# Performance work log

Measured on AMD Instinct MI355X. Metric: run time of the kernel, lower is better.

## Reference

```python
import jax, jax.numpy as jnp
import numpy as np


def _rnn_scan(x_pre, W_hh, b_hh, h0):
    # x_pre: [S, B, H] precomputed input projection; returns stacked h: [S, B, H]
    def step(h, xp):
        h = jnp.tanh(xp + h @ W_hh.T + b_hh)
        return h, h
    _, hs = jax.lax.scan(step, h0, x_pre)
    return hs


def setup_inputs() -> dict:
    key = jax.random.key(0)
    ks = jax.random.split(key, 12)
    B, S, E, H, V = 16, 256, 512, 1024, 32000
    sE, sH = 1.0 / np.sqrt(E), 1.0 / np.sqrt(H)
    return {
        "x_ids": jax.random.randint(ks[0], (B, S), 0, V),
        "emb": jax.random.normal(ks[1], (V, E), jnp.float32),
        "W_ih1": jax.random.normal(ks[2], (H, E), jnp.float32) * sE,
        "b_ih1": jax.random.normal(ks[3], (H,), jnp.float32) * sH,
        "W_hh1": jax.random.normal(ks[4], (H, H), jnp.float32) * sH,
        "b_hh1": jax.random.normal(ks[5], (H,), jnp.float32) * sH,
        "W_ih2": jax.random.normal(ks[6], (H, H), jnp.float32) * sH,
        "b_ih2": jax.random.normal(ks[7], (H,), jnp.float32) * sH,
        "W_hh2": jax.random.normal(ks[8], (H, H), jnp.float32) * sH,
        "b_hh2": jax.random.normal(ks[9], (H,), jnp.float32) * sH,
        "W_fc": jax.random.normal(ks[10], (V, H), jnp.float32) * sH,
        "b_fc": jax.random.normal(ks[11], (V,), jnp.float32) * sH,
    }


def reference(x_ids, emb, W_ih1, b_ih1, W_hh1, b_hh1, W_ih2, b_ih2, W_hh2, b_hh2, W_fc, b_fc):
    B, S = x_ids.shape
    H = W_hh1.shape[0]
    x = emb[x_ids]  # [B, S, E]
    # layer 1: precompute input projection for all steps, scan over time
    x1 = jnp.einsum('bse,he->sbh', x, W_ih1) + b_ih1  # [S, B, H]
    h0 = jnp.zeros((B, H), x.dtype)
    h1s = _rnn_scan(x1, W_hh1, b_hh1, h0)  # [S, B, H]
    # layer 2
    x2 = jnp.einsum('sbh,gh->sbg', h1s, W_ih2) + b_ih2
    h2s = _rnn_scan(x2, W_hh2, b_hh2, h0)  # [S, B, H]
    # per-step fc + softmax, vectorized
    logits = jnp.einsum('sbh,vh->bsv', h2s, W_fc) + b_fc  # [B, S, V]
    return jax.nn.softmax(logits, axis=-1)
```

## Files before the change

### kernel.cpp

```cpp
#include <hip/hip_runtime.h>
#include <cstdint>
#include <cstddef>

typedef unsigned short u16;
typedef __attribute__((ext_vector_type(4))) float f32x4;
typedef __attribute__((ext_vector_type(8))) short s16x8;
typedef __attribute__((ext_vector_type(8))) unsigned short u16x8;
typedef __attribute__((ext_vector_type(4))) unsigned short u16x4;

#define B_ 16
#define S_ 256
#define E_ 512
#define H_ 1024
#define V_ 32000
#define M_TOK (S_*B_)
#define BH (B_*H_)

__device__ __forceinline__ u16 f2bf(float f) {
  union { float f; unsigned u; } x; x.f = f;
  unsigned r = x.u + 0x7fffu + ((x.u >> 16) & 1u);
  return (u16)(r >> 16);
}
__device__ __forceinline__ float bf2f(u16 x) {
  union { unsigned u; float f; } c; c.u = ((unsigned)x) << 16; return c.f;
}

__device__ __forceinline__ void sc_load16(s16x8& d, const u16* p) {
  asm volatile("global_load_dwordx4 %0, %1, off sc0 sc1" : "=v"(d) : "v"(p));
}
__device__ __forceinline__ void sc_load8w(u16x4& d, const u16* p) {
  asm volatile("global_load_dwordx2 %0, %1, off sc0 sc1\n\ts_waitcnt vmcnt(0)"
               : "=v"(d) : "v"(p) : "memory");
}
__device__ __forceinline__ int sc_load4w(const int* p) {
  int d;
  asm volatile("global_load_dword %0, %1, off sc0 sc1\n\ts_waitcnt vmcnt(0)"
               : "=v"(d) : "v"(p) : "memory");
  return d;
}
__device__ __forceinline__ void sc_store8(u16* p, u16x4 v) {
  asm volatile("global_store_dwordx2 %0, %1, off sc0 sc1" :: "v"(p), "v"(v) : "memory");
}
__device__ __forceinline__ void sc_store4(int* p, int v) {
  asm volatile("global_store_dword %0, %1, off sc0 sc1" :: "v"(p), "v"(v) : "memory");
}
__device__ __forceinline__ void wait_vm0() {
  asm volatile("s_waitcnt vmcnt(0)" ::: "memory");
}

__global__ __launch_bounds__(256) void k_cvt(const float* __restrict__ src,
                                             u16* __restrict__ dst, int n4) {
  int i = blockIdx.x*blockDim.x + threadIdx.x;
  int stride = gridDim.x*blockDim.x;
  for (; i < n4; i += stride) {
    float4 v = reinterpret_cast<const float4*>(src)[i];
    ushort4 o;
    o.x = f2bf(v.x); o.y = f2bf(v.y); o.z = f2bf(v.z); o.w = f2bf(v.w);
    reinterpret_cast<ushort4*>(dst)[i] = o;
  }
}

__global__ __launch_bounds__(256) void k_embed(const int* __restrict__ ids,
                                               const float* __restrict__ emb,
                                               u16* __restrict__ A1) {
  int g = blockIdx.x*256 + threadIdx.x;
  int m = g >> 6;
  int c = g & 63;
  int s = m >> 4, b = m & 15;
  int id = ids[b*S_ + s];
  const float4* src = reinterpret_cast<const float4*>(emb + (size_t)id*E_ + (size_t)c*8);
  float4 v0 = src[0], v1 = src[1];
  u16x8 o;
  o[0]=f2bf(v0.x); o[1]=f2bf(v0.y); o[2]=f2bf(v0.z); o[3]=f2bf(v0.w);
  o[4]=f2bf(v1.x); o[5]=f2bf(v1.y); o[6]=f2bf(v1.z); o[7]=f2bf(v1.w);
  *reinterpret_cast<u16x8*>(A1 + (size_t)m*E_ + (size_t)c*8) = o;
}

#define BM 128
#define BN 128
#define BK 32

__device__ __forceinline__ void gload_lds16(const u16* g, u16* l) {
  __builtin_amdgcn_global_load_lds(
      (const __attribute__((address_space(1))) void*)g,
      (__attribute__((address_space(3))) void*)l,
      16, 0, 0);
}

template<int FCMODE>
__global__ __launch_bounds__(256)
void k_gemm(const u16* __restrict__ A, const u16* __restrict__ Bw,
            float* __restrict__ C, const float* __restrict__ bias,
            int M, int N, int K)
{
  __shared__ u16 lA[2][BM*BK];
  __shared__ u16 lB[2][BN*BK];
  const int tid = threadIdx.x;
  const int l = tid & 63, w = tid >> 6;

  const int nwg = gridDim.x * gridDim.y;
  int d = blockIdx.y * gridDim.x + blockIdx.x;
  int tt = (d & 7) * (nwg >> 3) + (d >> 3);
  const int n0 = (tt / gridDim.y) * BN;
  const int m0 = (tt % gridDim.y) * BM;

  const int wr = w >> 1, wc = w & 1;

  const int L0 = (w*2+0)*64 + l;
  const int L1 = (w*2+1)*64 + l;
  const int r0 = L0 >> 2, r1 = L1 >> 2;
  const int c0 = (L0 & 3) ^ ((r0 >> 1) & 3);
  const int c1 = (L1 & 3) ^ ((r1 >> 1) & 3);
  const u16* gA0 = A  + (size_t)(m0 + r0)*K + c0*8;
  const u16* gA1 = A  + (size_t)(m0 + r1)*K + c1*8;
  const u16* gB0 = Bw + (size_t)(n0 + r0)*K + c0*8;
  const u16* gB1 = Bw + (size_t)(n0 + r1)*K + c1*8;

  const int fr = l & 15;
  const int xc = (l >> 4) ^ ((fr >> 1) & 3);
  int aoff[4], boff[4];
#pragma unroll
  for (int f = 0; f < 4; ++f) {
    aoff[f] = (wr*64 + f*16 + fr) * BK + xc*8;
    boff[f] = (wc*64 + f*16 + fr) * BK + xc*8;
  }

  f32x4 acc[4][4] = {};
  const int KT = K / BK;

  gload_lds16(gA0, &lA[0][(w*2+0)*512]);
  gload_lds16(gA1, &lA[0][(w*2+1)*512]);
  gload_lds16(gB0, &lB[0][(w*2+0)*512]);
  gload_lds16(gB1, &lB[0][(w*2+1)*512]);
  __syncthreads();

  for (int kt = 0; kt < KT; ++kt) {
    const int buf = kt & 1;
    if (kt + 1 < KT) {
      const int koff = (kt+1)*BK;
      gload_lds16(gA0 + koff, &lA[buf^1][(w*2+0)*512]);
      gload_lds16(gA1 + koff, &lA[buf^1][(w*2+1)*512]);
      gload_lds16(gB0 + koff, &lB[buf^1][(w*2+0)*512]);
      gload_lds16(gB1 + koff, &lB[buf^1][(w*2+1)*512]);
    }
    s16x8 af[4], bq[4];
#pragma unroll
    for (int f = 0; f < 4; ++f) af[f] = *reinterpret_cast<const s16x8*>(&lA[buf][aoff[f]]);
#pragma unroll
    for (int f = 0; f < 4; ++f) bq[f] = *reinterpret_cast<const s16x8*>(&lB[buf][boff[f]]);
#pragma unroll
    for (int fm = 0; fm < 4; ++fm)
#pragma unroll
      for (int fn = 0; fn < 4; ++fn)
        acc[fm][fn] = __builtin_amdgcn_mfma_f32_16x16x32_bf16(af[fm], bq[fn], acc[fm][fn], 0, 0, 0);
    __syncthreads();
  }

  const int rowb = (l >> 4) * 4;
  const int colb = l & 15;
#pragma unroll
  for (int fm = 0; fm < 4; ++fm) {
#pragma unroll
    for (int fn = 0; fn < 4; ++fn) {
      const int col = n0 + wc*64 + fn*16 + colb;
#pragma unroll
      for (int r = 0; r < 4; ++r) {
        const int row = m0 + wr*64 + fm*16 + rowb + r;
        float v = acc[fm][fn][r];
        if (FCMODE == 1) {
          const int b = row & 15, s = row >> 4;
          C[((size_t)(b*S_ + s))*N + col] = v + bias[col];
        } else if (FCMODE == 2) {
          ((u16*)C)[(size_t)row*N + col] = f2bf(v);
        } else {
          C[(size_t)row*N + col] = v;
        }
      }
    }
  }
}

__global__ __launch_bounds__(256, 1)
void k_scan5(const u16* __restrict__ Whh1, const u16* __restrict__ Wih2,
             const u16* __restrict__ Whh2, const u16* __restrict__ x1b,
             const float* __restrict__ bih1, const float* __restrict__ bhh1,
             const float* __restrict__ bih2, const float* __restrict__ bhh2,
             u16* __restrict__ h1s, u16* __restrict__ u2s, u16* __restrict__ h2s,
             int* __restrict__ s1, int* __restrict__ su, int* __restrict__ s2)
{
  __shared__ u16 sh[BH];
  const int tid = threadIdx.x;
  const int l = tid & 63, w = tid >> 6;
  const int role = blockIdx.x >> 4;
  const int blk  = blockIdx.x & 15;
  const int rowA = blk*64 + w*16 + (l & 15);
  const int kc = l >> 4;
  const int bcol = l & 15;
  const int i0 = blk*64 + w*16 + kc*4;
  const int jme = (tid & 127) >> 3;

  const u16* Wsel = (role == 0) ? Whh1 : (role == 1) ? Wih2 : Whh2;
  s16x8 wf[32];
  {
    const u16* wp = Wsel + (size_t)rowA*H_ + kc*8;
#pragma unroll
    for (int ks = 0; ks < 32; ++ks) wf[ks] = *reinterpret_cast<const s16x8*>(wp + ks*32);
  }

  auto stage = [&](const u16* src, const int* sentrow) {
    while (sc_load4w(sentrow + jme) != 0) __builtin_amdgcn_s_sleep(2);
    s16x8 stg[8];
#pragma unroll
    for (int r = 0; r < 8; ++r) sc_load16(stg[r], src + (size_t)(tid + r*256)*8);
    wait_vm0();
#pragma unroll
    for (int r = 0; r < 8; ++r) {
      int idx8 = tid + r*256;
      int bt = idx8 >> 7, c8 = idx8 & 127;
      *reinterpret_cast<s16x8*>(reinterpret_cast<char*>(sh) +
          bt*2048 + ((c8*16) ^ ((bt & 7) << 4))) = stg[r];
    }
  };

  const int swz = (bcol & 7) << 4;
  auto hfrag = [&](int ks) -> s16x8 {
    return *reinterpret_cast<const s16x8*>(
        reinterpret_cast<const char*>(sh) + bcol*2048 + (((kc*16) + ks*64) ^ swz));
  };
  auto mfma32 = [&](f32x4& a0, f32x4& a1, f32x4& a2, f32x4& a3) {
#pragma unroll
    for (int ks = 0; ks < 32; ks += 4) {
      a0 = __builtin_amdgcn_mfma_f32_16x16x32_bf16(wf[ks+0], hfrag(ks+0), a0, 0, 0, 0);
      a1 = __builtin_amdgcn_mfma_f32_16x16x32_bf16(wf[ks+1], hfrag(ks+1), a1, 0, 0, 0);
      a2 = __builtin_amdgcn_mfma_f32_16x16x32_bf16(wf[ks+2], hfrag(ks+2), a2, 0, 0, 0);
      a3 = __builtin_amdgcn_mfma_f32_16x16x32_bf16(wf[ks+3], hfrag(ks+3), a3, 0, 0, 0);
    }
  };

  if (role == 0) {
    float bc[4];
#pragma unroll
    for (int r = 0; r < 4; ++r) bc[r] = bih1[i0+r] + bhh1[i0+r];
    for (int t = 0; t < S_; ++t) {
      f32x4 a0 = {}, a1 = {}, a2 = {}, a3 = {};
      if (t > 0) {
        stage(h1s + (size_t)(t-1)*BH, s1 + (t-1)*16);
        __syncthreads();
        mfma32(a0, a1, a2, a3);
      }
      u16x4 xr = *reinterpret_cast<const u16x4*>(x1b + (size_t)(t*B_ + bcol)*H_ + i0);
      f32x4 tot = (a0 + a1) + (a2 + a3);
      u16x4 o;
      o[0] = f2bf(tanhf(tot[0] + bf2f(xr[0]) + bc[0]));
      o[1] = f2bf(tanhf(tot[1] + bf2f(xr[1]) + bc[1]));
      o[2] = f2bf(tanhf(tot[2] + bf2f(xr[2]) + bc[2]));
      o[3] = f2bf(tanhf(tot[3] + bf2f(xr[3]) + bc[3]));
      sc_store8(h1s + (size_t)(t*B_ + bcol)*H_ + i0, o);
      wait_vm0();
      __syncthreads();
      if (tid == 0) sc_store4(s1 + t*16 + blk, 0);
    }
  } else if (role == 1) {
    float bc[4];
#pragma unroll
    for (int r = 0; r < 4; ++r) bc[r] = bih2[i0+r] + bhh2[i0+r];
    for (int t = 0; t < S_; ++t) {
      stage(h1s + (size_t)t*BH, s1 + t*16);
      __syncthreads();
      f32x4 a0 = {}, a1 = {}, a2 = {}, a3 = {};
      mfma32(a0, a1, a2, a3);
      f32x4 tot = (a0 + a1) + (a2 + a3);
      u16x4 o;
      o[0] = f2bf(tot[0] + bc[0]);
      o[1] = f2bf(tot[1] + bc[1]);
      o[2] = f2bf(tot[2] + bc[2]);
      o[3] = f2bf(tot[3] + bc[3]);
      sc_store8(u2s + (size_t)(t*B_ + bcol)*H_ + i0, o);
      wait_vm0();
      __syncthreads();
      if (tid == 0) sc_store4(su + t*16 + blk, 0);
    }
  } else {
    for (int t = 0; t < S_; ++t) {
      if (tid == 0) {
        while (sc_load4w(su + t*16 + blk) != 0) __builtin_amdgcn_s_sleep(2);
      }
      if (t > 0) stage(h2s + (size_t)(t-1)*BH, s2 + (t-1)*16);
      __syncthreads();
      u16x4 uv;
      sc_load8w(uv, u2s + (size_t)(t*B_ + bcol)*H_ + i0);
      f32x4 a0 = {}, a1 = {}, a2 = {}, a3 = {};
      if (t > 0) mfma32(a0, a1, a2, a3);
      f32x4 tot = (a0 + a1) + (a2 + a3);
      u16x4 o;
      o[0] = f2bf(tanhf(tot[0] + bf2f(uv[0])));
      o[1] = f2bf(tanhf(tot[1] + bf2f(uv[1])));
      o[2] = f2bf(tanhf(tot[2] + bf2f(uv[2])));
      o[3] = f2bf(tanhf(tot[3] + bf2f(uv[3])));
      sc_store8(h2s + (size_t)(t*B_ + bcol)*H_ + i0, o);
      wait_vm0();
      __syncthreads();
      if (tid == 0) sc_store4(s2 + t*16 + blk, 0);
    }
  }
}

__global__ __launch_bounds__(256)
void k_softmax(float* __restrict__ out) {
  const int gw = (blockIdx.x*256 + threadIdx.x) >> 6;
  const int l = threadIdx.x & 63;
  float* row = out + (size_t)gw*V_;
  float m = -3.4e38f, s = 0.f;
  for (int it = 0; it < 125; ++it) {
    float4 v = reinterpret_cast<const float4*>(row)[it*64 + l];
    float cm = fmaxf(fmaxf(v.x, v.y), fmaxf(v.z, v.w));
    float nm = fmaxf(m, cm);
    s = s*__expf(m - nm) + __expf(v.x-nm) + __expf(v.y-nm) + __expf(v.z-nm) + __expf(v.w-nm);
    m = nm;
  }
#pragma unroll
  for (int o = 32; o; o >>= 1) {
    float m2 = __shfl_xor(m, o), s2 = __shfl_xor(s, o);
    float nm = fmaxf(m, m2);
    s = s*__expf(m - nm) + s2*__expf(m2 - nm);
    m = nm;
  }
  const float inv = 1.f / s;
  for (int it = 0; it < 125; ++it) {
    float4 v = reinterpret_cast<const float4*>(row)[it*64 + l];
    float4 p;
    p.x = __expf(v.x - m)*inv; p.y = __expf(v.y - m)*inv;
    p.z = __expf(v.z - m)*inv; p.w = __expf(v.w - m)*inv;
    reinterpret_cast<float4*>(row)[it*64 + l] = p;
  }
}

extern "C" void kernel_launch(void* const* d_in, const int* in_sizes, int n_in,
                              void* d_out, int out_size, void* d_ws, size_t ws_size,
                              hipStream_t stream) {
  (void)in_sizes; (void)n_in; (void)out_size; (void)ws_size;
  const int*   x_ids = (const int*)  d_in[0];
  const float* emb   = (const float*)d_in[1];
  const float* Wih1  = (const float*)d_in[2];
  const float* bih1  = (const float*)d_in[3];
  const float* Whh1  = (const float*)d_in[4];
  const float* bhh1  = (const float*)d_in[5];
  const float* Wih2  = (const float*)d_in[6];
  const float* bih2  = (const float*)d_in[7];
  const float* Whh2  = (const float*)d_in[8];
  const float* bhh2  = (const float*)d_in[9];
  const float* Wfc   = (const float*)d_in[10];
  const float* bfc   = (const float*)d_in[11];
  float* out = (float*)d_out;

  char* ws = (char*)d_ws;
  size_t off = 0;
  auto alloc = [&](size_t bytes) {
    char* p = ws + off; off += (bytes + 255) & ~(size_t)255; return p;
  };
  int* sent   = (int*) alloc(3 * S_ * 16 * 4);
  u16* Wfcb   = (u16*) alloc((size_t)V_*H_*2);
  u16* Whh1b  = (u16*) alloc((size_t)H_*H_*2);
  u16* Wih2b  = (u16*) alloc((size_t)H_*H_*2);
  u16* Whh2b  = (u16*) alloc((size_t)H_*H_*2);
  u16* x1b    = (u16*) alloc((size_t)M_TOK*H_*2);
  u16* h1s    = (u16*) alloc((size_t)M_TOK*H_*2);
  u16* u2s    = (u16*) alloc((size_t)M_TOK*H_*2);
  u16* h2s    = (u16*) alloc((size_t)M_TOK*H_*2);
  u16* A1     = (u16*) alloc((size_t)M_TOK*E_*2);
  u16* Wih1b  = (u16*) alloc((size_t)H_*E_*2);
  int* s1 = sent, *su = sent + S_*16, *s2 = sent + 2*S_*16;

  k_cvt<<<256,  256, 0, stream>>>(Wih1, Wih1b, H_*E_/4);
  k_cvt<<<256,  256, 0, stream>>>(Whh1, Whh1b, H_*H_/4);
  k_cvt<<<256,  256, 0, stream>>>(Wih2, Wih2b, H_*H_/4);
  k_cvt<<<256,  256, 0, stream>>>(Whh2, Whh2b, H_*H_/4);
  k_cvt<<<2048, 256, 0, stream>>>(Wfc,  Wfcb,  V_*H_/4);
  k_embed<<<M_TOK*64/256, 256, 0, stream>>>(x_ids, emb, A1);

  k_gemm<2><<<dim3(H_/BN, M_TOK/BM), 256, 0, stream>>>(A1, Wih1b, (float*)x1b, nullptr, M_TOK, H_, E_);

  hipMemsetAsync(sent, 0xFF, 3 * S_ * 16 * 4, stream);
  k_scan5<<<48, 256, 0, stream>>>(Whh1b, Wih2b, Whh2b, x1b,
                                  bih1, bhh1, bih2, bhh2,
                                  h1s, u2s, h2s, s1, su, s2);

  k_gemm<1><<<dim3(V_/BN, M_TOK/BM), 256, 0, stream>>>(h2s, Wfcb, out, bfc, M_TOK, V_, H_);
  k_softmax<<<M_TOK/4, 256, 0, stream>>>(out);
}
```

Measured before the change: 1.935 ms.

## Use poisoned hidden-state data as flags and load fragments straight into registers

Drops the separate per-step sentinel arrays in the fused scan kernel. The h1/u2/h2 buffers are pre-filled with 0xFF, so every lane polls its own MFMA B-fragments straight from global memory until no all-ones dword remains. This removes the LDS staging, the block barriers, the vmcnt waits after each store and the flag stores from the serial per-timestep critical path. In exchange it adds three large memsets before the scan. Each wave now reads the full previous hidden state on its own, which multiplies L2 traffic per block.

```diff
diff --git a/kernel.cpp b/kernel.cpp
--- a/kernel.cpp
+++ b/kernel.cpp
@@ -7,6 +7,8 @@
 typedef __attribute__((ext_vector_type(8))) short s16x8;
 typedef __attribute__((ext_vector_type(8))) unsigned short u16x8;
 typedef __attribute__((ext_vector_type(4))) unsigned short u16x4;
+typedef __attribute__((ext_vector_type(4))) unsigned u32x4;
+typedef __attribute__((ext_vector_type(2))) unsigned u32x2;
 
 #define B_ 16
 #define S_ 256
@@ -25,24 +27,15 @@
   union { unsigned u; float f; } c; c.u = ((unsigned)x) << 16; return c.f;
 }
 
-__device__ __forceinline__ void sc_load16(s16x8& d, const u16* p) {
+__device__ __forceinline__ void sc_load16u(u32x4& d, const u16* p) {
   asm volatile("global_load_dwordx4 %0, %1, off sc0 sc1" : "=v"(d) : "v"(p));
 }
-__device__ __forceinline__ void sc_load8w(u16x4& d, const u16* p) {
+__device__ __forceinline__ void sc_load8u(u32x2& d, const u16* p) {
   asm volatile("global_load_dwordx2 %0, %1, off sc0 sc1\n\ts_waitcnt vmcnt(0)"
                : "=v"(d) : "v"(p) : "memory");
 }
-__device__ __forceinline__ int sc_load4w(const int* p) {
-  int d;
-  asm volatile("global_load_dword %0, %1, off sc0 sc1\n\ts_waitcnt vmcnt(0)"
-               : "=v"(d) : "v"(p) : "memory");
-  return d;
-}
 __device__ __forceinline__ void sc_store8(u16* p, u16x4 v) {
   asm volatile("global_store_dwordx2 %0, %1, off sc0 sc1" :: "v"(p), "v"(v) : "memory");
-}
-__device__ __forceinline__ void sc_store4(int* p, int v) {
-  asm volatile("global_store_dword %0, %1, off sc0 sc1" :: "v"(p), "v"(v) : "memory");
 }
 __device__ __forceinline__ void wait_vm0() {
   asm volatile("s_waitcnt vmcnt(0)" ::: "memory");
@@ -181,14 +174,12 @@
 }
 
 __global__ __launch_bounds__(256, 1)
-void k_scan5(const u16* __restrict__ Whh1, const u16* __restrict__ Wih2,
+void k_scan6(const u16* __restrict__ Whh1, const u16* __restrict__ Wih2,
              const u16* __restrict__ Whh2, const u16* __restrict__ x1b,
              const float* __restrict__ bih1, const float* __restrict__ bhh1,
              const float* __restrict__ bih2, const float* __restrict__ bhh2,
-             u16* __restrict__ h1s, u16* __restrict__ u2s, u16* __restrict__ h2s,
-             int* __restrict__ s1, int* __restrict__ su, int* __restrict__ s2)
+             u16* __restrict__ h1s, u16* __restrict__ u2s, u16* __restrict__ h2s)
 {
-  __shared__ u16 sh[BH];
   const int tid = threadIdx.x;
   const int l = tid & 63, w = tid >> 6;
   const int role = blockIdx.x >> 4;
@@ -197,7 +188,6 @@
   const int kc = l >> 4;
   const int bcol = l & 15;
   const int i0 = blk*64 + w*16 + kc*4;
-  const int jme = (tid & 127) >> 3;
 
   const u16* Wsel = (role == 0) ? Whh1 : (role == 1) ? Wih2 : Whh2;
   s16x8 wf[32];
@@ -207,33 +197,40 @@
     for (int ks = 0; ks < 32; ++ks) wf[ks] = *reinterpret_cast<const s16x8*>(wp + ks*32);
   }
 
-  auto stage = [&](const u16* src, const int* sentrow) {
-    while (sc_load4w(sentrow + jme) != 0) __builtin_amdgcn_s_sleep(2);
-    s16x8 stg[8];
-#pragma unroll
-    for (int r = 0; r < 8; ++r) sc_load16(stg[r], src + (size_t)(tid + r*256)*8);
+  u32x4 hf[32];
+
+  auto pollfrags = [&](const u16* hrow) {
+#pragma unroll
+    for (int ks = 0; ks < 32; ++ks) sc_load16u(hf[ks], hrow + ks*32);
     wait_vm0();
-#pragma unroll
-    for (int r = 0; r < 8; ++r) {
-      int idx8 = tid + r*256;
-      int bt = idx8 >> 7, c8 = idx8 & 127;
-      *reinterpret_cast<s16x8*>(reinterpret_cast<char*>(sh) +
-          bt*2048 + ((c8*16) ^ ((bt & 7) << 4))) = stg[r];
+    for (;;) {
+      unsigned M = 0;
+#pragma unroll
+      for (int ks = 0; ks < 32; ++ks) {
+        unsigned m0 = hf[ks][0] > hf[ks][1] ? hf[ks][0] : hf[ks][1];
+        unsigned m1 = hf[ks][2] > hf[ks][3] ? hf[ks][2] : hf[ks][3];
+        unsigned mm = m0 > m1 ? m0 : m1;
+        M = mm > M ? mm : M;
+      }
+      if (!__any(M == 0xFFFFFFFFu)) break;
+#pragma unroll
+      for (int ks = 0; ks < 32; ++ks) {
+        unsigned m0 = hf[ks][0] > hf[ks][1] ? hf[ks][0] : hf[ks][1];
+        unsigned m1 = hf[ks][2] > hf[ks][3] ? hf[ks][2] : hf[ks][3];
+        unsigned mm = m0 > m1 ? m0 : m1;
+        if (mm == 0xFFFFFFFFu) sc_load16u(hf[ks], hrow + ks*32);
+      }
+      wait_vm0();
     }
   };
 
-  const int swz = (bcol & 7) << 4;
-  auto hfrag = [&](int ks) -> s16x8 {
-    return *reinterpret_cast<const s16x8*>(
-        reinterpret_cast<const char*>(sh) + bcol*2048 + (((kc*16) + ks*64) ^ swz));
-  };
   auto mfma32 = [&](f32x4& a0, f32x4& a1, f32x4& a2, f32x4& a3) {
 #pragma unroll
     for (int ks = 0; ks < 32; ks += 4) {
-      a0 = __builtin_amdgcn_mfma_f32_16x16x32_bf16(wf[ks+0], hfrag(ks+0), a0, 0, 0, 0);
-      a1 = __builtin_amdgcn_mfma_f32_16x16x32_bf16(wf[ks+1], hfrag(ks+1), a1, 0, 0, 0);
-      a2 = __builtin_amdgcn_mfma_f32_16x16x32_bf16(wf[ks+2], hfrag(ks+2), a2, 0, 0, 0);
-      a3 = __builtin_amdgcn_mfma_f32_16x16x32_bf16(wf[ks+3], hfrag(ks+3), a3, 0, 0, 0);
+      a0 = __builtin_amdgcn_mfma_f32_16x16x32_bf16(wf[ks+0], __builtin_bit_cast(s16x8, hf[ks+0]), a0, 0, 0, 0);
+      a1 = __builtin_amdgcn_mfma_f32_16x16x32_bf16(wf[ks+1], __builtin_bit_cast(s16x8, hf[ks+1]), a1, 0, 0, 0);
+      a2 = __builtin_amdgcn_mfma_f32_16x16x32_bf16(wf[ks+2], __builtin_bit_cast(s16x8, hf[ks+2]), a2, 0, 0, 0);
+      a3 = __builtin_amdgcn_mfma_f32_16x16x32_bf16(wf[ks+3], __builtin_bit_cast(s16x8, hf[ks+3]), a3, 0, 0, 0);
     }
   };
 
@@ -242,13 +239,12 @@
 #pragma unroll
     for (int r = 0; r < 4; ++r) bc[r] = bih1[i0+r] + bhh1[i0+r];
     for (int t = 0; t < S_; ++t) {
+      u16x4 xr = *reinterpret_cast<const u16x4*>(x1b + (size_t)(t*B_ + bcol)*H_ + i0);
       f32x4 a0 = {}, a1 = {}, a2 = {}, a3 = {};
       if (t > 0) {
-        stage(h1s + (size_t)(t-1)*BH, s1 + (t-1)*16);
-        __syncthreads();
+        pollfrags(h1s + ((size_t)(t-1)*B_ + bcol)*H_ + kc*8);
         mfma32(a0, a1, a2, a3);
       }
-      u16x4 xr = *reinterpret_cast<const u16x4*>(x1b + (size_t)(t*B_ + bcol)*H_ + i0);
       f32x4 tot = (a0 + a1) + (a2 + a3);
       u16x4 o;
       o[0] = f2bf(tanhf(tot[0] + bf2f(xr[0]) + bc[0]));
@@ -256,17 +252,13 @@
       o[2] = f2bf(tanhf(tot[2] + bf2f(xr[2]) + bc[2]));
       o[3] = f2bf(tanhf(tot[3] + bf2f(xr[3]) + bc[3]));
       sc_store8(h1s + (size_t)(t*B_ + bcol)*H_ + i0, o);
-      wait_vm0();
-      __syncthreads();
-      if (tid == 0) sc_store4(s1 + t*16 + blk, 0);
     }
   } else if (role == 1) {
     float bc[4];
 #pragma unroll
     for (int r = 0; r < 4; ++r) bc[r] = bih2[i0+r] + bhh2[i0+r];
     for (int t = 0; t < S_; ++t) {
-      stage(h1s + (size_t)t*BH, s1 + t*16);
-      __syncthreads();
+      pollfrags(h1s + ((size_t)t*B_ + bcol)*H_ + kc*8);
       f32x4 a0 = {}, a1 = {}, a2 = {}, a3 = {};
       mfma32(a0, a1, a2, a3);
       f32x4 tot = (a0 + a1) + (a2 + a3);
@@ -276,31 +268,26 @@
       o[2] = f2bf(tot[2] + bc[2]);
       o[3] = f2bf(tot[3] + bc[3]);
       sc_store8(u2s + (size_t)(t*B_ + bcol)*H_ + i0, o);
-      wait_vm0();
-      __syncthreads();
-      if (tid == 0) sc_store4(su + t*16 + blk, 0);
     }
   } else {
     for (int t = 0; t < S_; ++t) {
-      if (tid == 0) {
-        while (sc_load4w(su + t*16 + blk) != 0) __builtin_amdgcn_s_sleep(2);
-      }
-      if (t > 0) stage(h2s + (size_t)(t-1)*BH, s2 + (t-1)*16);
-      __syncthreads();
-      u16x4 uv;
-      sc_load8w(uv, u2s + (size_t)(t*B_ + bcol)*H_ + i0);
+      const u16* up = u2s + (size_t)(t*B_ + bcol)*H_ + i0;
       f32x4 a0 = {}, a1 = {}, a2 = {}, a3 = {};
+      if (t > 0) {
+        pollfrags(h2s + ((size_t)(t-1)*B_ + bcol)*H_ + kc*8);
+      }
+      u32x2 uv;
+      sc_load8u(uv, up);
+      while ((uv[0] > uv[1] ? uv[0] : uv[1]) == 0xFFFFFFFFu) sc_load8u(uv, up);
+      u16x4 uq = __builtin_bit_cast(u16x4, uv);
       if (t > 0) mfma32(a0, a1, a2, a3);
       f32x4 tot = (a0 + a1) + (a2 + a3);
       u16x4 o;
-      o[0] = f2bf(tanhf(tot[0] + bf2f(uv[0])));
-      o[1] = f2bf(tanhf(tot[1] + bf2f(uv[1])));
-      o[2] = f2bf(tanhf(tot[2] + bf2f(uv[2])));
-      o[3] = f2bf(tanhf(tot[3] + bf2f(uv[3])));
+      o[0] = f2bf(tanhf(tot[0] + bf2f(uq[0])));
+      o[1] = f2bf(tanhf(tot[1] + bf2f(uq[1])));
+      o[2] = f2bf(tanhf(tot[2] + bf2f(uq[2])));
+      o[3] = f2bf(tanhf(tot[3] + bf2f(uq[3])));
       sc_store8(h2s + (size_t)(t*B_ + bcol)*H_ + i0, o);
-      wait_vm0();
-      __syncthreads();
-      if (tid == 0) sc_store4(s2 + t*16 + blk, 0);
     }
   }
 }
@@ -358,7 +345,6 @@
   auto alloc = [&](size_t bytes) {
     char* p = ws + off; off += (bytes + 255) & ~(size_t)255; return p;
   };
-  int* sent   = (int*) alloc(3 * S_ * 16 * 4);
   u16* Wfcb   = (u16*) alloc((size_t)V_*H_*2);
   u16* Whh1b  = (u16*) alloc((size_t)H_*H_*2);
   u16* Wih2b  = (u16*) alloc((size_t)H_*H_*2);
@@ -369,7 +355,6 @@
   u16* h2s    = (u16*) alloc((size_t)M_TOK*H_*2);
   u16* A1     = (u16*) alloc((size_t)M_TOK*E_*2);
   u16* Wih1b  = (u16*) alloc((size_t)H_*E_*2);
-  int* s1 = sent, *su = sent + S_*16, *s2 = sent + 2*S_*16;
 
   k_cvt<<<256,  256, 0, stream>>>(Wih1, Wih1b, H_*E_/4);
   k_cvt<<<256,  256, 0, stream>>>(Whh1, Whh1b, H_*H_/4);
@@ -380,10 +365,11 @@
 
   k_gemm<2><<<dim3(H_/BN, M_TOK/BM), 256, 0, stream>>>(A1, Wih1b, (float*)x1b, nullptr, M_TOK, H_, E_);
 
-  hipMemsetAsync(sent, 0xFF, 3 * S_ * 16 * 4, stream);
-  k_scan5<<<48, 256, 0, stream>>>(Whh1b, Wih2b, Whh2b, x1b,
-                                  bih1, bhh1, bih2, bhh2,
-                                  h1s, u2s, h2s, s1, su, s2);
+  hipMemsetAsync(h1s, 0xFF, (size_t)M_TOK*H_*2, stream);
+  hipMemsetAsync(u2s, 0xFF, (size_t)M_TOK*H_*2, stream);
+  hipMemsetAsync(h2s, 0xFF, (size_t)M_TOK*H_*2, stream);
+  k_scan6<<<48, 256, 0, stream>>>(Whh1b, Wih2b, Whh2b, x1b,
+                                  bih1, bhh1, bih2, bhh2, h1s, u2s, h2s);
 
   k_gemm<1><<<dim3(V_/BN, M_TOK/BM), 256, 0, stream>>>(h2s, Wfcb, out, bfc, M_TOK, V_, H_);
   k_softmax<<<M_TOK/4, 256, 0, stream>>>(out);
```

Measured after the change: 2.503 ms. 29.3% more time.

## Overlap FC GEMM tiles with RNN scan in a persistent megakernel

Applied to the files above, without the earlier changes.

Merges the recurrent scan and the output FC GEMM into one launch. The 48 scan blocks publish per-block progress of layer 2, and the FC tile blocks wait on that progress with a bounded spin before computing their tile, so the FC work can run on idle CUs while the scan is still going. Tiles that time out are marked not done and are recomputed by a cleanup kernel. This risks FC blocks taking CU slots or memory bandwidth from the scan blocks, adds spin-wait traffic, and relies on the scan blocks being scheduled first, since block dispatch order is not guaranteed.

```diff
diff --git a/kernel.cpp b/kernel.cpp
--- a/kernel.cpp
+++ b/kernel.cpp
@@ -7,6 +7,7 @@
 typedef __attribute__((ext_vector_type(8))) short s16x8;
 typedef __attribute__((ext_vector_type(8))) unsigned short u16x8;
 typedef __attribute__((ext_vector_type(4))) unsigned short u16x4;
+typedef __attribute__((ext_vector_type(4))) unsigned u32x4;
 
 #define B_ 16
 #define S_ 256
@@ -15,6 +16,8 @@
 #define V_ 32000
 #define M_TOK (S_*B_)
 #define BH (B_*H_)
+#define NT_FC 250
+#define MT_FC 32
 
 __device__ __forceinline__ u16 f2bf(float f) {
   union { float f; unsigned u; } x; x.f = f;
@@ -26,6 +29,9 @@
 }
 
 __device__ __forceinline__ void sc_load16(s16x8& d, const u16* p) {
+  asm volatile("global_load_dwordx4 %0, %1, off sc0 sc1" : "=v"(d) : "v"(p));
+}
+__device__ __forceinline__ void sc_load16u(u32x4& d, const u16* p) {
   asm volatile("global_load_dwordx4 %0, %1, off sc0 sc1" : "=v"(d) : "v"(p));
 }
 __device__ __forceinline__ void sc_load8w(u16x4& d, const u16* p) {
@@ -167,10 +173,7 @@
       for (int r = 0; r < 4; ++r) {
         const int row = m0 + wr*64 + fm*16 + rowb + r;
         float v = acc[fm][fn][r];
-        if (FCMODE == 1) {
-          const int b = row & 15, s = row >> 4;
-          C[((size_t)(b*S_ + s))*N + col] = v + bias[col];
-        } else if (FCMODE == 2) {
+        if (FCMODE == 2) {
           ((u16*)C)[(size_t)row*N + col] = f2bf(v);
         } else {
           C[(size_t)row*N + col] = v;
@@ -180,129 +183,267 @@
   }
 }
 
-__global__ __launch_bounds__(256, 1)
-void k_scan5(const u16* __restrict__ Whh1, const u16* __restrict__ Wih2,
-             const u16* __restrict__ Whh2, const u16* __restrict__ x1b,
-             const float* __restrict__ bih1, const float* __restrict__ bhh1,
-             const float* __restrict__ bih2, const float* __restrict__ bhh2,
-             u16* __restrict__ h1s, u16* __restrict__ u2s, u16* __restrict__ h2s,
-             int* __restrict__ s1, int* __restrict__ su, int* __restrict__ s2)
+__device__ __forceinline__ void fc_tile(const u16* __restrict__ A, const u16* __restrict__ Bw,
+                                        float* __restrict__ C, const float* __restrict__ bias,
+                                        int m0, int n0, u16* smem)
 {
-  __shared__ u16 sh[BH];
   const int tid = threadIdx.x;
   const int l = tid & 63, w = tid >> 6;
-  const int role = blockIdx.x >> 4;
-  const int blk  = blockIdx.x & 15;
-  const int rowA = blk*64 + w*16 + (l & 15);
-  const int kc = l >> 4;
-  const int bcol = l & 15;
-  const int i0 = blk*64 + w*16 + kc*4;
-  const int jme = (tid & 127) >> 3;
-
-  const u16* Wsel = (role == 0) ? Whh1 : (role == 1) ? Wih2 : Whh2;
-  s16x8 wf[32];
-  {
-    const u16* wp = Wsel + (size_t)rowA*H_ + kc*8;
-#pragma unroll
-    for (int ks = 0; ks < 32; ++ks) wf[ks] = *reinterpret_cast<const s16x8*>(wp + ks*32);
-  }
-
-  auto stage = [&](const u16* src, const int* sentrow) {
-    while (sc_load4w(sentrow + jme) != 0) __builtin_amdgcn_s_sleep(2);
-    s16x8 stg[8];
-#pragma unroll
-    for (int r = 0; r < 8; ++r) sc_load16(stg[r], src + (size_t)(tid + r*256)*8);
-    wait_vm0();
-#pragma unroll
-    for (int r = 0; r < 8; ++r) {
-      int idx8 = tid + r*256;
-      int bt = idx8 >> 7, c8 = idx8 & 127;
-      *reinterpret_cast<s16x8*>(reinterpret_cast<char*>(sh) +
-          bt*2048 + ((c8*16) ^ ((bt & 7) << 4))) = stg[r];
-    }
-  };
-
-  const int swz = (bcol & 7) << 4;
-  auto hfrag = [&](int ks) -> s16x8 {
-    return *reinterpret_cast<const s16x8*>(
-        reinterpret_cast<const char*>(sh) + bcol*2048 + (((kc*16) + ks*64) ^ swz));
-  };
-  auto mfma32 = [&](f32x4& a0, f32x4& a1, f32x4& a2, f32x4& a3) {
-#pragma unroll
-    for (int ks = 0; ks < 32; ks += 4) {
-      a0 = __builtin_amdgcn_mfma_f32_16x16x32_bf16(wf[ks+0], hfrag(ks+0), a0, 0, 0, 0);
-      a1 = __builtin_amdgcn_mfma_f32_16x16x32_bf16(wf[ks+1], hfrag(ks+1), a1, 0, 0, 0);
-      a2 = __builtin_amdgcn_mfma_f32_16x16x32_bf16(wf[ks+2], hfrag(ks+2), a2, 0, 0, 0);
-      a3 = __builtin_amdgcn_mfma_f32_16x16x32_bf16(wf[ks+3], hfrag(ks+3), a3, 0, 0, 0);
-    }
-  };
-
-  if (role == 0) {
-    float bc[4];
-#pragma unroll
-    for (int r = 0; r < 4; ++r) bc[r] = bih1[i0+r] + bhh1[i0+r];
-    for (int t = 0; t < S_; ++t) {
-      f32x4 a0 = {}, a1 = {}, a2 = {}, a3 = {};
-      if (t > 0) {
-        stage(h1s + (size_t)(t-1)*BH, s1 + (t-1)*16);
+  const int wr = w >> 1, wc = w & 1;
+  u16* lA = smem;
+  u16* lB = smem + 8192;
+
+  const int L0 = (w*2+0)*64 + l;
+  const int L1 = (w*2+1)*64 + l;
+  const int r0 = L0 >> 2, r1 = L1 >> 2;
+  const int c0 = (L0 & 3) ^ ((r0 >> 1) & 3);
+  const int c1 = (L1 & 3) ^ ((r1 >> 1) & 3);
+  const u16* gA0 = A  + (size_t)(m0 + r0)*H_ + c0*8;
+  const u16* gA1 = A  + (size_t)(m0 + r1)*H_ + c1*8;
+  const u16* gB0 = Bw + (size_t)(n0 + r0)*H_ + c0*8;
+  const u16* gB1 = Bw + (size_t)(n0 + r1)*H_ + c1*8;
+
+  const int fr = l & 15;
+  const int xc = (l >> 4) ^ ((fr >> 1) & 3);
+  int aoff[4], boff[4];
+#pragma unroll
+  for (int f = 0; f < 4; ++f) {
+    aoff[f] = (wr*64 + f*16 + fr) * BK + xc*8;
+    boff[f] = (wc*64 + f*16 + fr) * BK + xc*8;
+  }
+
+  f32x4 acc[4][4] = {};
+
+  gload_lds16(gA0, lA + (w*2+0)*512);
+  gload_lds16(gA1, lA + (w*2+1)*512);
+  gload_lds16(gB0, lB + (w*2+0)*512);
+  gload_lds16(gB1, lB + (w*2+1)*512);
+  __syncthreads();
+
+  for (int kt = 0; kt < 32; ++kt) {
+    const int buf = kt & 1;
+    if (kt + 1 < 32) {
+      const int koff = (kt+1)*BK;
+      gload_lds16(gA0 + koff, lA + (buf^1)*4096 + (w*2+0)*512);
+      gload_lds16(gA1 + koff, lA + (buf^1)*4096 + (w*2+1)*512);
+      gload_lds16(gB0 + koff, lB + (buf^1)*4096 + (w*2+0)*512);
+      gload_lds16(gB1 + koff, lB + (buf^1)*4096 + (w*2+1)*512);
+    }
+    s16x8 af[4], bq[4];
+#pragma unroll
+    for (int f = 0; f < 4; ++f) af[f] = *reinterpret_cast<const s16x8*>(lA + buf*4096 + aoff[f]);
+#pragma unroll
+    for (int f = 0; f < 4; ++f) bq[f] = *reinterpret_cast<const s16x8*>(lB + buf*4096 + boff[f]);
+#pragma unroll
+    for (int fm = 0; fm < 4; ++fm)
+#pragma unroll
+      for (int fn = 0; fn < 4; ++fn)
+        acc[fm][fn] = __builtin_amdgcn_mfma_f32_16x16x32_bf16(af[fm], bq[fn], acc[fm][fn], 0, 0, 0);
+    __syncthreads();
+  }
+
+  const int rowb = (l >> 4) * 4;
+  const int colb = l & 15;
+#pragma unroll
+  for (int fm = 0; fm < 4; ++fm) {
+#pragma unroll
+    for (int fn = 0; fn < 4; ++fn) {
+      const int col = n0 + wc*64 + fn*16 + colb;
+      const float bv = bias[col];
+#pragma unroll
+      for (int r = 0; r < 4; ++r) {
+        const int row = m0 + wr*64 + fm*16 + rowb + r;
+        const int b = row & 15, s = row >> 4;
+        C[((size_t)(b*S_ + s))*V_ + col] = acc[fm][fn][r] + bv;
+      }
+    }
+  }
+}
+
+__global__ __launch_bounds__(256)
+void k_mega(const u16* __restrict__ Whh1, const u16* __restrict__ Wih2,
+            const u16* __restrict__ Whh2, const u16* __restrict__ x1b,
+            const float* __restrict__ bih1, const float* __restrict__ bhh1,
+            const float* __restrict__ bih2, const float* __restrict__ bhh2,
+            u16* __restrict__ h1s, u16* __restrict__ u2s, u16* __restrict__ h2s,
+            int* __restrict__ s1, int* __restrict__ su, int* __restrict__ s2,
+            const u16* __restrict__ Wfcb, const float* __restrict__ bfc,
+            float* __restrict__ out, int* __restrict__ prog2, int* __restrict__ done)
+{
+  __shared__ u16 smem[16384];
+  const int bid = blockIdx.x;
+  const int tid = threadIdx.x;
+
+  if (bid < 48) {
+    const int l = tid & 63, w = tid >> 6;
+    const int role = bid >> 4;
+    const int blk  = bid & 15;
+    const int rowA = blk*64 + w*16 + (l & 15);
+    const int kc = l >> 4;
+    const int bcol = l & 15;
+    const int i0 = blk*64 + w*16 + kc*4;
+    const int jme = (tid & 127) >> 3;
+
+    const u16* Wsel = (role == 0) ? Whh1 : (role == 1) ? Wih2 : Whh2;
+    s16x8 wf[32];
+    {
+      const u16* wp = Wsel + (size_t)rowA*H_ + kc*8;
+#pragma unroll
+      for (int ks = 0; ks < 32; ++ks) wf[ks] = *reinterpret_cast<const s16x8*>(wp + ks*32);
+    }
+
+    auto stage = [&](const u16* src, const int* sentrow) {
+      while (sc_load4w(sentrow + jme) != 0) __builtin_amdgcn_s_sleep(2);
+      s16x8 stg[8];
+#pragma unroll
+      for (int r = 0; r < 8; ++r) sc_load16(stg[r], src + (size_t)(tid + r*256)*8);
+      wait_vm0();
+#pragma unroll
+      for (int r = 0; r < 8; ++r) {
+        int idx8 = tid + r*256;
+        int bt = idx8 >> 7, c8 = idx8 & 127;
+        *reinterpret_cast<s16x8*>(reinterpret_cast<char*>(smem) +
+            bt*2048 + ((c8*16) ^ ((bt & 7) << 4))) = stg[r];
+      }
+    };
+
+    const int swz = (bcol & 7) << 4;
+    auto hfrag = [&](int ks) -> s16x8 {
+      return *reinterpret_cast<const s16x8*>(
+          reinterpret_cast<const char*>(smem) + bcol*2048 + (((kc*16) + ks*64) ^ swz));
+    };
+    auto mfma32 = [&](f32x4& a0, f32x4& a1, f32x4& a2, f32x4& a3) {
+#pragma unroll
+      for (int ks = 0; ks < 32; ks += 4) {
+        a0 = __builtin_amdgcn_mfma_f32_16x16x32_bf16(wf[ks+0], hfrag(ks+0), a0, 0, 0, 0);
+        a1 = __builtin_amdgcn_mfma_f32_16x16x32_bf16(wf[ks+1], hfrag(ks+1), a1, 0, 0, 0);
+        a2 = __builtin_amdgcn_mfma_f32_16x16x32_bf16(wf[ks+2], hfrag(ks+2), a2, 0, 0, 0);
+        a3 = __builtin_amdgcn_mfma_f32_16x16x32_bf16(wf[ks+3], hfrag(ks+3), a3, 0, 0, 0);
+      }
+    };
+
+    if (role == 0) {
+      float bc[4];
+#pragma unroll
+      for (int r = 0; r < 4; ++r) bc[r] = bih1[i0+r] + bhh1[i0+r];
+      for (int t = 0; t < S_; ++t) {
+        f32x4 a0 = {}, a1 = {}, a2 = {}, a3 = {};
+        if (t > 0) {
+          stage(h1s + (size_t)(t-1)*BH, s1 + (t-1)*16);
+          __syncthreads();
+          mfma32(a0, a1, a2, a3);
+        }
+        u16x4 xr = *reinterpret_cast<const u16x4*>(x1b + (size_t)(t*B_ + bcol)*H_ + i0);
+        f32x4 tot = (a0 + a1) + (a2 + a3);
+        u16x4 o;
+        o[0] = f2bf(tanhf(tot[0] + bf2f(xr[0]) + bc[0]));
+        o[1] = f2bf(tanhf(tot[1] + bf2f(xr[1]) + bc[1]));
+        o[2] = f2bf(tanhf(tot[2] + bf2f(xr[2]) + bc[2]));
+        o[3] = f2bf(tanhf(tot[3] + bf2f(xr[3]) + bc[3]));
+        sc_store8(h1s + (size_t)(t*B_ + bcol)*H_ + i0, o);
+        wait_vm0();
         __syncthreads();
+        if (tid == 0) sc_store4(s1 + t*16 + blk, 0);
+      }
+    } else if (role == 1) {
+      float bc[4];
+#pragma unroll
+      for (int r = 0; r < 4; ++r) bc[r] = bih2[i0+r] + bhh2[i0+r];
+      for (int t = 0; t < S_; ++t) {
+        stage(h1s + (size_t)t*BH, s1 + t*16);
+        __syncthreads();
+        f32x4 a0 = {}, a1 = {}, a2 = {}, a3 = {};
         mfma32(a0, a1, a2, a3);
-      }
-      u16x4 xr = *reinterpret_cast<const u16x4*>(x1b + (size_t)(t*B_ + bcol)*H_ + i0);
-      f32x4 tot = (a0 + a1) + (a2 + a3);
-      u16x4 o;
-      o[0] = f2bf(tanhf(tot[0] + bf2f(xr[0]) + bc[0]));
-      o[1] = f2bf(tanhf(tot[1] + bf2f(xr[1]) + bc[1]));
-      o[2] = f2bf(tanhf(tot[2] + bf2f(xr[2]) + bc[2]));
-      o[3] = f2bf(tanhf(tot[3] + bf2f(xr[3]) + bc[3]));
-      sc_store8(h1s + (size_t)(t*B_ + bcol)*H_ + i0, o);
+        f32x4 tot = (a0 + a1) + (a2 + a3);
+        u16x4 o;
+        o[0] = f2bf(tot[0] + bc[0]);
+        o[1] = f2bf(tot[1] + bc[1]);
+        o[2] = f2bf(tot[2] + bc[2]);
+        o[3] = f2bf(tot[3] + bc[3]);
+        sc_store8(u2s + (size_t)(t*B_ + bcol)*H_ + i0, o);
+        wait_vm0();
+        __syncthreads();
+        if (tid == 0) sc_store4(su + t*16 + blk, 0);
+      }
+    } else {
+      for (int t = 0; t < S_; ++t) {
+        if (tid == 0) {
+          while (sc_load4w(su + t*16 + blk) != 0) __builtin_amdgcn_s_sleep(2);
+        }
+        if (t > 0) stage(h2s + (size_t)(t-1)*BH, s2 + (t-1)*16);
+        __syncthreads();
+        u16x4 uv;
+        sc_load8w(uv, u2s + (size_t)(t*B_ + bcol)*H_ + i0);
+        f32x4 a0 = {}, a1 = {}, a2 = {}, a3 = {};
+        if (t > 0) mfma32(a0, a1, a2, a3);
+        f32x4 tot = (a0 + a1) + (a2 + a3);
+        u16x4 o;
+        o[0] = f2bf(tanhf(tot[0] + bf2f(uv[0])));
+        o[1] = f2bf(tanhf(tot[1] + bf2f(uv[1])));
+        o[2] = f2bf(tanhf(tot[2] + bf2f(uv[2])));
+        o[3] = f2bf(tanhf(tot[3] + bf2f(uv[3])));
+        sc_store8(h2s + (size_t)(t*B_ + bcol)*H_ + i0, o);
+        wait_vm0();
+        __syncthreads();
+        if (tid == 0) {
+          sc_store4(s2 + t*16 + blk, 0);
+          sc_store4(prog2 + blk, t + 1);
+        }
+      }
+    }
+    return;
+  }
+
+  const int q = bid - 48;
+  if (q >= MT_FC * NT_FC) return;
+  const int mt = q / NT_FC;
+  const int nt = q - mt * NT_FC;
+  const unsigned need = (unsigned)((mt + 1) * 8);
+
+  __shared__ int s_ok;
+  if (tid == 0) {
+    int ok = 0;
+    const u16* pp = (const u16*)prog2;
+    for (int it = 0; it < 2500; ++it) {
+      u32x4 pa, pb, pc, pd;
+      sc_load16u(pa, pp); sc_load16u(pb, pp + 8);
+      sc_load16u(pc, pp + 16); sc_load16u(pd, pp + 24);
       wait_vm0();
-      __syncthreads();
-      if (tid == 0) sc_store4(s1 + t*16 + blk, 0);
-    }
-  } else if (role == 1) {
-    float bc[4];
-#pragma unroll
-    for (int r = 0; r < 4; ++r) bc[r] = bih2[i0+r] + bhh2[i0+r];
-    for (int t = 0; t < S_; ++t) {
-      stage(h1s + (size_t)t*BH, s1 + t*16);
-      __syncthreads();
-      f32x4 a0 = {}, a1 = {}, a2 = {}, a3 = {};
-      mfma32(a0, a1, a2, a3);
-      f32x4 tot = (a0 + a1) + (a2 + a3);
-      u16x4 o;
-      o[0] = f2bf(tot[0] + bc[0]);
-      o[1] = f2bf(tot[1] + bc[1]);
-      o[2] = f2bf(tot[2] + bc[2]);
-      o[3] = f2bf(tot[3] + bc[3]);
-      sc_store8(u2s + (size_t)(t*B_ + bcol)*H_ + i0, o);
-      wait_vm0();
-      __syncthreads();
-      if (tid == 0) sc_store4(su + t*16 + blk, 0);
-    }
-  } else {
-    for (int t = 0; t < S_; ++t) {
-      if (tid == 0) {
-        while (sc_load4w(su + t*16 + blk) != 0) __builtin_amdgcn_s_sleep(2);
-      }
-      if (t > 0) stage(h2s + (size_t)(t-1)*BH, s2 + (t-1)*16);
-      __syncthreads();
-      u16x4 uv;
-      sc_load8w(uv, u2s + (size_t)(t*B_ + bcol)*H_ + i0);
-      f32x4 a0 = {}, a1 = {}, a2 = {}, a3 = {};
-      if (t > 0) mfma32(a0, a1, a2, a3);
-      f32x4 tot = (a0 + a1) + (a2 + a3);
-      u16x4 o;
-      o[0] = f2bf(tanhf(tot[0] + bf2f(uv[0])));
-      o[1] = f2bf(tanhf(tot[1] + bf2f(uv[1])));
-      o[2] = f2bf(tanhf(tot[2] + bf2f(uv[2])));
-      o[3] = f2bf(tanhf(tot[3] + bf2f(uv[3])));
-      sc_store8(h2s + (size_t)(t*B_ + bcol)*H_ + i0, o);
-      wait_vm0();
-      __syncthreads();
-      if (tid == 0) sc_store4(s2 + t*16 + blk, 0);
-    }
-  }
+      unsigned m0 = pa[0] < pa[1] ? pa[0] : pa[1];
+      unsigned m1 = pa[2] < pa[3] ? pa[2] : pa[3];
+      unsigned m2 = pb[0] < pb[1] ? pb[0] : pb[1];
+      unsigned m3 = pb[2] < pb[3] ? pb[2] : pb[3];
+      unsigned m4 = pc[0] < pc[1] ? pc[0] : pc[1];
+      unsigned m5 = pc[2] < pc[3] ? pc[2] : pc[3];
+      unsigned m6 = pd[0] < pd[1] ? pd[0] : pd[1];
+      unsigned m7 = pd[2] < pd[3] ? pd[2] : pd[3];
+      m0 = m0 < m1 ? m0 : m1;  m2 = m2 < m3 ? m2 : m3;
+      m4 = m4 < m5 ? m4 : m5;  m6 = m6 < m7 ? m6 : m7;
+      m0 = m0 < m2 ? m0 : m2;  m4 = m4 < m6 ? m4 : m6;
+      unsigned mn = m0 < m4 ? m0 : m4;
+      if (mn >= need) { ok = 1; break; }
+      __builtin_amdgcn_s_sleep(32);
+    }
+    s_ok = ok;
+  }
+  __syncthreads();
+  if (!s_ok) return;
+
+  fc_tile(h2s, Wfcb, out, bfc, mt*BM, nt*BN, smem);
+  if (tid == 0) done[q] = 1;
+}
+
+__global__ __launch_bounds__(256)
+void k_fc_cleanup(const u16* __restrict__ h2s, const u16* __restrict__ Wfcb,
+                  const float* __restrict__ bfc, float* __restrict__ out,
+                  const int* __restrict__ done)
+{
+  __shared__ u16 smem[16384];
+  const int q = blockIdx.x;
+  if (done[q]) return;
+  const int mt = q / NT_FC;
+  const int nt = q - mt * NT_FC;
+  fc_tile(h2s, Wfcb, out, bfc, mt*BM, nt*BN, smem);
 }
 
 __global__ __launch_bounds__(256)
@@ -359,6 +500,7 @@
     char* p = ws + off; off += (bytes + 255) & ~(size_t)255; return p;
   };
   int* sent   = (int*) alloc(3 * S_ * 16 * 4);
+  int* ctrl   = (int*) alloc(64 + MT_FC*NT_FC*4);
   u16* Wfcb   = (u16*) alloc((size_t)V_*H_*2);
   u16* Whh1b  = (u16*) alloc((size_t)H_*H_*2);
   u16* Wih2b  = (u16*) alloc((size_t)H_*H_*2);
@@ -370,6 +512,8 @@
   u16* A1     = (u16*) alloc((size_t)M_TOK*E_*2);
   u16* Wih1b  = (u16*) alloc((size_t)H_*E_*2);
   int* s1 = sent, *su = sent + S_*16, *s2 = sent + 2*S_*16;
+  int* prog2 = ctrl;
+  int* done  = ctrl + 16;
 
   k_cvt<<<256,  256, 0, stream>>>(Wih1, Wih1b, H_*E_/4);
   k_cvt<<<256,  256, 0, stream>>>(Whh1, Whh1b, H_*H_/4);
@@ -381,10 +525,12 @@
   k_gemm<2><<<dim3(H_/BN, M_TOK/BM), 256, 0, stream>>>(A1, Wih1b, (float*)x1b, nullptr, M_TOK, H_, E_);
 
   hipMemsetAsync(sent, 0xFF, 3 * S_ * 16 * 4, stream);
-  k_scan5<<<48, 256, 0, stream>>>(Whh1b, Wih2b, Whh2b, x1b,
-                                  bih1, bhh1, bih2, bhh2,
-                                  h1s, u2s, h2s, s1, su, s2);
-
-  k_gemm<1><<<dim3(V_/BN, M_TOK/BM), 256, 0, stream>>>(h2s, Wfcb, out, bfc, M_TOK, V_, H_);
+  hipMemsetAsync(ctrl, 0, 64 + MT_FC*NT_FC*4, stream);
+
+  k_mega<<<48 + MT_FC*NT_FC, 256, 0, stream>>>(
+      Whh1b, Wih2b, Whh2b, x1b, bih1, bhh1, bih2, bhh2,
+      h1s, u2s, h2s, s1, su, s2, Wfcb, bfc, out, prog2, done);
+
+  k_fc_cleanup<<<MT_FC*NT_FC, 256, 0, stream>>>(h2s, Wfcb, bfc, out, done);
   k_softmax<<<M_TOK/4, 256, 0, stream>>>(out);
 }
```

Result: faster. 1.646 ms (-14.9%).
